# Performance work log

Hardware: AMD Instinct MI355X
Metric: run time of the kernel (lower is better)

## Reference

```python
import jax, jax.numpy as jnp
import numpy as np

B, S, H = 1, 2048, 2048
E, K, I = 8, 2, 1024   # n_routed_experts, num_experts_per_tok, moe_intermediate_size
IS = 2 * I             # shared experts intermediate = moe_intermediate_size * n_shared_experts


def setup_inputs() -> dict:
    key = jax.random.key(0)
    ks = jax.random.split(key, 8)
    w = 0.02  # weight scale so gate softmax is not degenerate
    return {
        "x": jax.random.normal(ks[0], (B, S, H), jnp.float32),
        "gate_w": jax.random.normal(ks[1], (E, H), jnp.float32) * w,
        "wg": jax.random.normal(ks[2], (E, H, I), jnp.float32) * w,
        "wu": jax.random.normal(ks[3], (E, H, I), jnp.float32) * w,
        "wd": jax.random.normal(ks[4], (E, I, H), jnp.float32) * w,
        "sg": jax.random.normal(ks[5], (H, IS), jnp.float32) * w,
        "su": jax.random.normal(ks[6], (H, IS), jnp.float32) * w,
        "sd": jax.random.normal(ks[7], (IS, H), jnp.float32) * w,
    }


def reference(x, gate_w, wg, wu, wd, sg, su, sd):
    b, s, h = x.shape
    xf = x.reshape(-1, h)                                  # [T, H]
    T = xf.shape[0]

    # ---- gate: softmax scores, top-k, renormalize ----
    scores = jax.nn.softmax(jnp.einsum("th,eh->te", xf, gate_w), axis=-1)  # [T, E]
    topk_w, topk_i = jax.lax.top_k(scores, K)              # sorted descending
    topk_w = topk_w / jnp.sum(topk_w, axis=-1, keepdims=True)

    # dense combine weights [T, E] (indices unique per token)
    cw = jnp.zeros_like(scores).at[jnp.arange(T)[:, None], topk_i].add(topk_w)

    # ---- routed experts: SwiGLU MLP per expert, weighted combine ----
    g = jnp.einsum("th,ehi->eti", xf, wg)                  # [E, T, I]
    u = jnp.einsum("th,ehi->eti", xf, wu)
    hgated = jax.nn.silu(g) * u
    eo = jnp.einsum("eti,eih->eth", hgated, wd)            # [E, T, H]
    y = jnp.einsum("te,eth->th", cw, eo)                   # [T, H]

    # ---- shared experts ----
    shared = (jax.nn.silu(xf @ sg) * (xf @ su)) @ sd       # [T, H]

    return (y + shared).reshape(b, s, h)
```

## Files before the change

### kernel.cpp

```cpp
#include <hip/hip_runtime.h>


typedef unsigned short u16;
typedef unsigned int   u32;
typedef __bf16 bf16x8 __attribute__((ext_vector_type(8)));
typedef float  f32x4  __attribute__((ext_vector_type(4)));

#define T_TOK 2048
#define HDIM  2048
#define IDIM  1024
#define NEXP  8
#define ISDIM 2048
#define MAXROWS 5120

__device__ __forceinline__ u16 f2bf(float f) {
  u32 x = __float_as_uint(f);
  return (u16)((x + 0x7FFFu + ((x >> 16) & 1u)) >> 16);
}
__device__ __forceinline__ float bf2f(u16 v) { return __uint_as_float(((u32)v) << 16); }

#define GLL(g, l)                                                              \
  __builtin_amdgcn_global_load_lds(                                            \
      (const __attribute__((address_space(1))) void*)(g),                      \
      (__attribute__((address_space(3))) void*)(l), 16, 0, 0)

__global__ void init_kernel(int* __restrict__ perm, int* __restrict__ meta,
                            int* __restrict__ zrow) {
  int idx = blockIdx.x * 256 + threadIdx.x;
  if (idx < 8192) perm[idx] = -1;
  if (idx < 16) meta[idx] = 0;
  if (idx < 1024) zrow[idx] = 0;
}

__global__ __launch_bounds__(256) void gate_kernel(
    const float* __restrict__ x, const float* __restrict__ gw,
    u16* __restrict__ xb, float* __restrict__ outz,
    float* __restrict__ topw, int* __restrict__ topi, int* __restrict__ meta) {
  const int t = blockIdx.x, tid = threadIdx.x;
  const long o = (long)t * HDIM + tid * 8;
  float4 a = *(const float4*)(x + o);
  float4 b = *(const float4*)(x + o + 4);
  float4 z = {0.f, 0.f, 0.f, 0.f};
  *(float4*)(outz + o) = z;
  *(float4*)(outz + o + 4) = z;
  uint4 w;
  w.x = (u32)f2bf(a.x) | ((u32)f2bf(a.y) << 16);
  w.y = (u32)f2bf(a.z) | ((u32)f2bf(a.w) << 16);
  w.z = (u32)f2bf(b.x) | ((u32)f2bf(b.y) << 16);
  w.w = (u32)f2bf(b.z) | ((u32)f2bf(b.w) << 16);
  *(uint4*)(xb + o) = w;
  float acc[NEXP];
#pragma unroll
  for (int e = 0; e < NEXP; e++) {
    const float* gr = gw + e * HDIM + tid * 8;
    float4 wa = *(const float4*)gr;
    float4 wb = *(const float4*)(gr + 4);
    acc[e] = a.x * wa.x + a.y * wa.y + a.z * wa.z + a.w * wa.w +
             b.x * wb.x + b.y * wb.y + b.z * wb.z + b.w * wb.w;
  }
#pragma unroll
  for (int off = 32; off; off >>= 1)
#pragma unroll
    for (int e = 0; e < NEXP; e++) acc[e] += __shfl_down(acc[e], off, 64);
  __shared__ float red[4][NEXP];
  if ((tid & 63) == 0) {
#pragma unroll
    for (int e = 0; e < NEXP; e++) red[tid >> 6][e] = acc[e];
  }
  __syncthreads();
  if (tid == 0) {
    float s[NEXP];
#pragma unroll
    for (int e = 0; e < NEXP; e++) s[e] = red[0][e] + red[1][e] + red[2][e] + red[3][e];
    int i0 = 0;
#pragma unroll
    for (int e = 1; e < NEXP; e++)
      if (s[e] > s[i0]) i0 = e;
    int i1 = -1;
#pragma unroll
    for (int e = 0; e < NEXP; e++) {
      if (e == i0) continue;
      if (i1 < 0 || s[e] > s[i1]) i1 = e;
    }
    float w0 = 1.f / (1.f + __expf(s[i1] - s[i0]));
    topw[t * 2 + 0] = w0;
    topw[t * 2 + 1] = 1.f - w0;
    topi[t * 2 + 0] = i0;
    topi[t * 2 + 1] = i1;
    atomicAdd(meta + i0, 1);
    atomicAdd(meta + i1, 1);
  }
}

__global__ void scan_kernel(int* __restrict__ meta) {
  if (threadIdx.x == 0 && blockIdx.x == 0) {
    int o = 0;
    meta[16] = 0;
#pragma unroll
    for (int e = 0; e < NEXP; e++) {
      o += (meta[e] + 127) & ~127;
      meta[17 + e] = o;
    }
  }
}

__global__ void assign_kernel(const int* __restrict__ topi, int* __restrict__ meta,
                              int* __restrict__ perm, int* __restrict__ tokrow) {
  int idx = blockIdx.x * 256 + threadIdx.x;
  int e = topi[idx];
  int pos = atomicAdd(meta + 8 + e, 1);
  int row = meta[16 + e] + pos;
  perm[row] = idx;
  tokrow[idx] = row;
}

__device__ __forceinline__ void tcast_tile(const float* __restrict__ in,
                                           u16* __restrict__ out, int R, int C) {
  __shared__ float tile[64 * 65];
  int r0 = blockIdx.y * 64, c0 = blockIdx.x * 64;
  int t = threadIdx.x;
  int i = t >> 4, j4 = t & 15;
#pragma unroll
  for (int ii = 0; ii < 4; ii++) {
    int r = i + ii * 16;
    float4 v = *(const float4*)(in + (long)(r0 + r) * C + c0 + j4 * 4);
    tile[r * 65 + j4 * 4 + 0] = v.x;
    tile[r * 65 + j4 * 4 + 1] = v.y;
    tile[r * 65 + j4 * 4 + 2] = v.z;
    tile[r * 65 + j4 * 4 + 3] = v.w;
  }
  __syncthreads();
  int cc = t >> 3, rr = (t & 7) * 8;
#pragma unroll
  for (int pp = 0; pp < 2; pp++) {
    int c = cc + pp * 32;
    u16 e[8];
#pragma unroll
    for (int u = 0; u < 8; u++) e[u] = f2bf(tile[(rr + u) * 65 + c]);
    uint4 w;
    w.x = (u32)e[0] | ((u32)e[1] << 16);
    w.y = (u32)e[2] | ((u32)e[3] << 16);
    w.z = (u32)e[4] | ((u32)e[5] << 16);
    w.w = (u32)e[6] | ((u32)e[7] << 16);
    *(uint4*)(out + (long)(c0 + c) * R + r0 + rr) = w;
  }
}

__global__ __launch_bounds__(256) void tcast_kernel(const float* __restrict__ in,
                                                    u16* __restrict__ out, int R, int C,
                                                    long inz, long outz) {
  tcast_tile(in + (long)blockIdx.z * inz, out + (long)blockIdx.z * outz, R, C);
}

__global__ __launch_bounds__(256) void tcast2_kernel(
    const float* __restrict__ inA, const float* __restrict__ inB,
    u16* __restrict__ out, int R, int C, long inz, long outz, long boff, int zsplit) {
  int z = blockIdx.z;
  const float* in;
  u16* o;
  if (z < zsplit) {
    in = inA + (long)z * inz;
    o = out + (long)z * outz;
  } else {
    int e = z - zsplit;
    in = inB + (long)e * inz;
    o = out + (long)e * outz + boff;
  }
  tcast_tile(in, o, R, C);
}

template <int HALF8>
__device__ __forceinline__ void silu_do(u16* __restrict__ buf, long i) {
  long r = i / HALF8, c = i % HALF8;
  u16* g = buf + r * (long)HALF8 * 16 + c * 8;
  uint4 gv = *(const uint4*)g;
  uint4 uv = *(const uint4*)(g + HALF8 * 8);
  const u32* gp = &gv.x;
  const u32* up = &uv.x;
  uint4 w;
  u32* wp = &w.x;
#pragma unroll
  for (int j = 0; j < 4; j++) {
    float g0 = bf2f((u16)(gp[j] & 0xFFFF)), g1 = bf2f((u16)(gp[j] >> 16));
    float u0 = bf2f((u16)(up[j] & 0xFFFF)), u1 = bf2f((u16)(up[j] >> 16));
    float r0 = g0 / (1.f + __expf(-g0)) * u0;
    float r1 = g1 / (1.f + __expf(-g1)) * u1;
    wp[j] = (u32)f2bf(r0) | ((u32)f2bf(r1) << 16);
  }
  *(uint4*)g = w;
}

template <int HALF8>
__global__ void silu_kernel(u16* __restrict__ buf) {
  long i = (long)blockIdx.x * 256 + threadIdx.x;
  silu_do<HALF8>(buf, i);
}

__global__ void silu2_kernel(u16* __restrict__ gur, u16* __restrict__ gus) {
  const long NR = (long)MAXROWS * IDIM / 8;
  long i = (long)blockIdx.x * 256 + threadIdx.x;
  if (i < NR)
    silu_do<128>(gur, i);
  else
    silu_do<256>(gus, i - NR);
}

template <int CMODE , bool PERMA, bool SEGB>
__device__ __forceinline__ void gemm_body2(
    int mt, int nt, u16* lds, const u16* __restrict__ A, long lda,
    const u16* __restrict__ B, long ldbz, int K, u16* __restrict__ Cb,
    float* __restrict__ Cf, long ldc, const int* __restrict__ offp,
    const int* __restrict__ perm, const u16* __restrict__ zrow) {
  const int row0 = mt * 128;
  if constexpr (SEGB) {
    if (row0 >= offp[8]) return;
    int e = 0;
    while (offp[e + 1] <= row0) ++e;
    B += (long)e * ldbz;
  }
  const int tid = threadIdx.x;

  const int ra = tid >> 2, sa = tid & 3;
  const u16* gA;
  if constexpr (PERMA) {
    int p = perm[row0 + ra];
    gA = ((p < 0) ? zrow : A + (long)(p >> 1) * lda) + (sa ^ ((ra >> 1) & 3)) * 8;
  } else {
    gA = A + (long)(row0 + ra) * lda + (sa ^ ((ra >> 1) & 3)) * 8;
  }
  const int rb0 = ra, rb1 = ra + 128;
  const u16* gB0 = B + (long)(nt * 256 + rb0) * K + (sa ^ ((rb0 >> 1) & 3)) * 8;
  const u16* gB1 = B + (long)(nt * 256 + rb1) * K + (sa ^ ((rb1 >> 1) & 3)) * 8;
  const int dAo = tid * 8;
  const int dBo = 4096 + tid * 8;

  const int lane = tid & 63, w = tid >> 6;
  const int wm = (w >> 2) * 64, wn = (w & 3) * 64;
  const int lrow = lane & 15, kc = lane >> 4;
  int offA[4], offB[4];
#pragma unroll
  for (int i = 0; i < 4; i++) {
    int rA = wm + i * 16 + lrow;
    offA[i] = rA * 32 + (kc ^ ((rA >> 1) & 3)) * 8;
    int rB = wn + i * 16 + lrow;
    offB[i] = 4096 + rB * 32 + (kc ^ ((rB >> 1) & 3)) * 8;
  }

  f32x4 acc[4][4];
#pragma unroll
  for (int i = 0; i < 4; i++)
#pragma unroll
    for (int j = 0; j < 4; j++) acc[i][j] = f32x4{0.f, 0.f, 0.f, 0.f};

  const int nk = K >> 5;
  {
    u16* b0 = lds;
    GLL(gA, b0 + dAo);
    GLL(gB0, b0 + dBo);
    GLL(gB1, b0 + dBo + 4096);
    u16* b1 = lds + 12288;
    GLL(gA + 32, b1 + dAo);
    GLL(gB0 + 32, b1 + dBo);
    GLL(gB1 + 32, b1 + dBo + 4096);
  }
  int cur = 0, stg = 2;
  for (int t = 0; t < nk; ++t) {
    asm volatile("s_waitcnt vmcnt(3)" ::: "memory");
    __builtin_amdgcn_s_barrier();
    u16* buf = lds + cur * 12288;
    bf16x8 af[4], bfv[4];
#pragma unroll
    for (int i = 0; i < 4; i++) af[i] = *(const bf16x8*)(buf + offA[i]);
#pragma unroll
    for (int i = 0; i < 4; i++) bfv[i] = *(const bf16x8*)(buf + offB[i]);
    int t2 = t + 2;
    if (t2 >= nk) t2 -= nk;
    {
      u16* sb = lds + stg * 12288;
      const int kk = t2 * 32;
      GLL(gA + kk, sb + dAo);
      GLL(gB0 + kk, sb + dBo);
      GLL(gB1 + kk, sb + dBo + 4096);
    }
    __builtin_amdgcn_s_barrier();
    __builtin_amdgcn_s_setprio(1);
#pragma unroll
    for (int mi = 0; mi < 4; mi++)
#pragma unroll
      for (int ni = 0; ni < 4; ni++)
        acc[mi][ni] = __builtin_amdgcn_mfma_f32_16x16x32_bf16(af[mi], bfv[ni],
                                                              acc[mi][ni], 0, 0, 0);
    __builtin_amdgcn_s_setprio(0);
    cur = (cur == 2) ? 0 : cur + 1;
    stg = (stg == 2) ? 0 : stg + 1;
  }
  asm volatile("s_waitcnt vmcnt(0)" ::: "memory");

  const int crow = row0 + wm + ((lane >> 4) << 2);
  const int ccol = nt * 256 + wn + (lane & 15);
#pragma unroll
  for (int mi = 0; mi < 4; mi++) {
#pragma unroll
    for (int ni = 0; ni < 4; ni++) {
#pragma unroll
      for (int r = 0; r < 4; r++) {
        int row = crow + mi * 16 + r;
        int col = ccol + ni * 16;
        float v = acc[mi][ni][r];
        if constexpr (CMODE == 0) {
          Cb[(long)row * ldc + col] = f2bf(v);
        } else {
          Cf[(long)row * ldc + col] = v;
        }
      }
    }
  }
}

__global__ __launch_bounds__(512, 4) void gemm_gu_fused(
    const u16* __restrict__ xb, const u16* __restrict__ wguT,
    const u16* __restrict__ sgsuT, u16* __restrict__ gur, u16* __restrict__ gus,
    const int* __restrict__ offp, const int* __restrict__ perm,
    const u16* __restrict__ zrow) {
  __shared__ __align__(16) u16 lds2[36864];
  int bid = blockIdx.x;
  if (bid < 320) {
    gemm_body2<0, true, true>(bid >> 3, bid & 7, lds2, xb, HDIM, wguT,
                              (long)2 * IDIM * HDIM, HDIM, gur, nullptr, 2 * IDIM,
                              offp, perm, zrow);
  } else {
    int b = bid - 320;
    gemm_body2<0, false, false>(b >> 4, b & 15, lds2, xb, HDIM, sgsuT, 0, HDIM, gus,
                                nullptr, 2 * ISDIM, nullptr, nullptr, nullptr);
  }
}

__global__ __launch_bounds__(512, 4) void gemm_down_plain(
    const u16* __restrict__ gus, const u16* __restrict__ sdT,
    const u16* __restrict__ gur, const u16* __restrict__ wdT, float* __restrict__ out,
    u16* __restrict__ eo, const int* __restrict__ offp) {
  __shared__ __align__(16) u16 lds2[36864];
  int bid = blockIdx.x;
  if (bid < 128) {
    gemm_body2<1, false, false>(bid >> 3, bid & 7, lds2, gus, 2 * ISDIM, sdT, 0, ISDIM,
                                nullptr, out, HDIM, nullptr, nullptr, nullptr);
  } else {
    int b = bid - 128;
    gemm_body2<0, false, true>(b >> 3, b & 7, lds2, gur, 2 * IDIM, wdT,
                               (long)HDIM * IDIM, IDIM, eo, nullptr, HDIM, offp,
                               nullptr, nullptr);
  }
}

__global__ __launch_bounds__(256) void combine_kernel(float* __restrict__ out,
                                                      const u16* __restrict__ eo,
                                                      const int* __restrict__ tokrow,
                                                      const float* __restrict__ topw) {
  const int t = blockIdx.x, tid = threadIdx.x;
  const long o = (long)t * HDIM + tid * 8;
  const int r0 = tokrow[t * 2], r1 = tokrow[t * 2 + 1];
  const float w0 = topw[t * 2], w1 = topw[t * 2 + 1];
  float4 a = *(const float4*)(out + o);
  float4 b = *(const float4*)(out + o + 4);
  uint4 e0 = *(const uint4*)(eo + (long)r0 * HDIM + tid * 8);
  uint4 e1 = *(const uint4*)(eo + (long)r1 * HDIM + tid * 8);
  const u32* p0 = &e0.x;
  const u32* p1 = &e1.x;
  float r[8] = {a.x, a.y, a.z, a.w, b.x, b.y, b.z, b.w};
#pragma unroll
  for (int j = 0; j < 4; j++) {
    r[j * 2 + 0] += w0 * bf2f((u16)(p0[j] & 0xFFFF)) + w1 * bf2f((u16)(p1[j] & 0xFFFF));
    r[j * 2 + 1] += w0 * bf2f((u16)(p0[j] >> 16)) + w1 * bf2f((u16)(p1[j] >> 16));
  }
  float4 oa = {r[0], r[1], r[2], r[3]};
  float4 ob = {r[4], r[5], r[6], r[7]};
  *(float4*)(out + o) = oa;
  *(float4*)(out + o + 4) = ob;
}

template <int CMODE, bool PERMA, bool SEGB>
__device__ __forceinline__ void gemm_body(
    int mt, int nt, u16* ldsA, u16* ldsB, const u16* __restrict__ A, long lda,
    const u16* __restrict__ B, long ldbz, int K, u16* __restrict__ Cb,
    float* __restrict__ Cf, long ldc, const int* __restrict__ offp,
    const int* __restrict__ perm, const float* __restrict__ topw,
    const u16* __restrict__ zrow) {
  const int row0 = mt * 128;
  if constexpr (SEGB) {
    if (row0 >= offp[8]) return;
    int e = 0;
    while (offp[e + 1] <= row0) ++e;
    B += (long)e * ldbz;
  }
  const int tid = threadIdx.x;
  const u16* gA[4];
  const u16* gB[4];
  u16 *lA[4], *lB[4];
#pragma unroll
  for (int j = 0; j < 4; j++) {
    int c = tid + 256 * j;
    int r = c >> 3, s = c & 7;
    int gk = (s ^ (r & 7)) * 8;
    const u16* arow;
    if constexpr (PERMA) {
      int p = perm[row0 + r];
      arow = (p < 0) ? zrow : A + (long)(p >> 1) * lda;
    } else {
      arow = A + (long)(row0 + r) * lda;
    }
    gA[j] = arow + gk;
    gB[j] = B + (long)(nt * 128 + r) * K + gk;
    lA[j] = ldsA + c * 8;
    lB[j] = ldsB + c * 8;
  }
  const int lane = tid & 63, wave = tid >> 6;
  const int wm = (wave & 1) * 64, wn = (wave >> 1) * 64;
  const int lrow = lane & 15;
  const int kchunk = lane >> 4;
  const int rsw = lrow & 7;

  f32x4 acc[4][4];
#pragma unroll
  for (int i = 0; i < 4; i++)
#pragma unroll
    for (int j = 0; j < 4; j++) acc[i][j] = f32x4{0.f, 0.f, 0.f, 0.f};

  const int nk = K >> 6;
  for (int kt = 0; kt < nk; ++kt) {
    const int kk = kt * 64;
#pragma unroll
    for (int j = 0; j < 4; j++) {
      GLL(gA[j] + kk, lA[j]);
      GLL(gB[j] + kk, lB[j]);
    }
    __syncthreads();
#pragma unroll
    for (int half = 0; half < 2; half++) {
      const int slot = (kchunk + half * 4) ^ rsw;
      bf16x8 af[4], bfv[4];
#pragma unroll
      for (int mi = 0; mi < 4; mi++)
        af[mi] = *(const bf16x8*)(ldsA + (wm + lrow + mi * 16) * 64 + slot * 8);
#pragma unroll
      for (int ni = 0; ni < 4; ni++)
        bfv[ni] = *(const bf16x8*)(ldsB + (wn + lrow + ni * 16) * 64 + slot * 8);
#pragma unroll
      for (int mi = 0; mi < 4; mi++)
#pragma unroll
        for (int ni = 0; ni < 4; ni++)
          acc[mi][ni] = __builtin_amdgcn_mfma_f32_16x16x32_bf16(af[mi], bfv[ni],
                                                                acc[mi][ni], 0, 0, 0);
    }
    __syncthreads();
  }

  const int crow = row0 + wm + ((lane >> 4) << 2);
  const int ccol = nt * 128 + wn + (lane & 15);
#pragma unroll
  for (int mi = 0; mi < 4; mi++) {
#pragma unroll
    for (int ni = 0; ni < 4; ni++) {
#pragma unroll
      for (int r = 0; r < 4; r++) {
        int row = crow + mi * 16 + r;
        int col = ccol + ni * 16;
        float v = acc[mi][ni][r];
        if constexpr (CMODE == 0) {
          Cb[(long)row * ldc + col] = f2bf(v);
        } else if constexpr (CMODE == 1) {
          Cf[(long)row * ldc + col] = v;
        } else if constexpr (CMODE == 2) {
          int p = perm[row];
          if (p >= 0) atomicAdd(Cf + (long)(p >> 1) * ldc + col, topw[p] * v);
        } else {
          atomicAdd(Cf + (long)row * ldc + col, v);
        }
      }
    }
  }
}

__global__ __launch_bounds__(256) void gemm_routed_gu(
    const u16* __restrict__ xb, const u16* __restrict__ wT, u16* __restrict__ Cb,
    const int* __restrict__ offp, const int* __restrict__ perm,
    const u16* __restrict__ zrow) {
  __shared__ __align__(16) u16 ldsA[8192], ldsB[8192];
  gemm_body<0, true, true>(blockIdx.y, blockIdx.x, ldsA, ldsB, xb, HDIM, wT,
                           (long)IDIM * HDIM, HDIM, Cb, nullptr, 2 * IDIM, offp, perm,
                           nullptr, zrow);
}
__global__ __launch_bounds__(256) void gemm_shared_gu(const u16* __restrict__ xb,
                                                      const u16* __restrict__ sgsuT,
                                                      u16* __restrict__ gus) {
  __shared__ __align__(16) u16 ldsA[8192], ldsB[8192];
  gemm_body<0, false, false>(blockIdx.y, blockIdx.x, ldsA, ldsB, xb, HDIM, sgsuT, 0, HDIM,
                             gus, nullptr, 2 * ISDIM, nullptr, nullptr, nullptr, nullptr);
}
__global__ __launch_bounds__(256) void gemm_down_atomic(
    const u16* __restrict__ gus, const u16* __restrict__ sdT,
    const u16* __restrict__ gur, const u16* __restrict__ wdT, float* __restrict__ out,
    const int* __restrict__ offp, const int* __restrict__ perm,
    const float* __restrict__ topw) {
  __shared__ __align__(16) u16 ldsA[8192], ldsB[8192];
  int bid = blockIdx.x;
  if (bid < 256) {
    gemm_body<3, false, false>(bid / 16, bid % 16, ldsA, ldsB, gus, 2 * ISDIM, sdT, 0,
                               ISDIM, nullptr, out, HDIM, nullptr, nullptr, nullptr,
                               nullptr);
  } else {
    int b = bid - 256;
    gemm_body<2, false, true>(b / 16, b % 16, ldsA, ldsB, gur, 2 * IDIM, wdT,
                              (long)HDIM * IDIM, IDIM, nullptr, out, HDIM, offp, perm,
                              topw, nullptr);
  }
}

extern "C" void kernel_launch(void* const* d_in, const int* in_sizes, int n_in,
                              void* d_out, int out_size, void* d_ws, size_t ws_size,
                              hipStream_t stream) {
  const float* x  = (const float*)d_in[0];
  const float* gw = (const float*)d_in[1];
  const float* wg = (const float*)d_in[2];
  const float* wu = (const float*)d_in[3];
  const float* wd = (const float*)d_in[4];
  const float* sg = (const float*)d_in[5];
  const float* su = (const float*)d_in[6];
  const float* sd = (const float*)d_in[7];
  float* out = (float*)d_out;

  char* ws = (char*)d_ws;
  size_t off = 0;
  auto alloc = [&](size_t b) {
    size_t o = off;
    off += (b + 255) & ~(size_t)255;
    return (void*)(ws + o);
  };
  u16*   xb     = (u16*)alloc((size_t)T_TOK * HDIM * 2);
  u16*   gur    = (u16*)alloc((size_t)MAXROWS * 2 * IDIM * 2);
  u16*   gus    = (u16*)alloc((size_t)T_TOK * 2 * ISDIM * 2);
  float* topw   = (float*)alloc((size_t)T_TOK * 2 * 4);
  int*   topi   = (int*)alloc((size_t)T_TOK * 2 * 4);
  int*   tokrow = (int*)alloc((size_t)T_TOK * 2 * 4);
  int*   perm   = (int*)alloc(8192 * 4);
  int*   meta   = (int*)alloc(64 * 4);
  u16*   zrow   = (u16*)alloc(4096);
  size_t base = off;

  const size_t SZ_WGUT  = (size_t)NEXP * 2 * IDIM * HDIM * 2;
  const size_t SZ_SGSUT = (size_t)2 * ISDIM * HDIM * 2;
  const size_t SZ_SDT   = (size_t)HDIM * ISDIM * 2;
  const size_t SZ_WDT   = (size_t)NEXP * HDIM * IDIM * 2;
  const bool fused = ws_size >= base + SZ_WGUT + SZ_SGSUT;

  init_kernel<<<32, 256, 0, stream>>>(perm, meta, (int*)zrow);
  gate_kernel<<<T_TOK, 256, 0, stream>>>(x, gw, xb, out, topw, topi, meta);
  scan_kernel<<<1, 64, 0, stream>>>(meta);
  assign_kernel<<<16, 256, 0, stream>>>(topi, meta, perm, tokrow);

  if (fused) {
    u16* wguT  = (u16*)(ws + base);
    u16* sgsuT = (u16*)(ws + base + SZ_WGUT);
    u16* sdT   = wguT;
    u16* wdT   = wguT + SZ_SDT / 2;
    u16* eo    = wguT + (SZ_SDT + SZ_WDT) / 2;
    tcast2_kernel<<<dim3(IDIM / 64, HDIM / 64, 2 * NEXP), 256, 0, stream>>>(
        wg, wu, wguT, HDIM, IDIM, (long)HDIM * IDIM, (long)2 * IDIM * HDIM,
        (long)IDIM * HDIM, NEXP);
    tcast2_kernel<<<dim3(ISDIM / 64, HDIM / 64, 2), 256, 0, stream>>>(
        sg, su, sgsuT, HDIM, ISDIM, 0, 0, (long)ISDIM * HDIM, 1);
    gemm_gu_fused<<<576, 512, 0, stream>>>(xb, wguT, sgsuT, gur, gus, meta + 16, perm,
                                           zrow);
    silu2_kernel<<<(MAXROWS * IDIM / 8 + T_TOK * ISDIM / 8) / 256, 256, 0, stream>>>(
        gur, gus);
    tcast_kernel<<<dim3(HDIM / 64, ISDIM / 64, 1), 256, 0, stream>>>(sd, sdT, ISDIM,
                                                                     HDIM, 0, 0);
    tcast_kernel<<<dim3(HDIM / 64, IDIM / 64, NEXP), 256, 0, stream>>>(
        wd, wdT, IDIM, HDIM, (long)IDIM * HDIM, (long)HDIM * IDIM);
    gemm_down_plain<<<448, 512, 0, stream>>>(gus, sdT, gur, wdT, out, eo, meta + 16);
    combine_kernel<<<T_TOK, 256, 0, stream>>>(out, eo, tokrow, topw);
  } else {
    u16* wT    = (u16*)(ws + base);
    u16* sgsuT = wT;
    u16* sdT   = wT;
    u16* wdT   = wT + SZ_SDT / 2;
    tcast_kernel<<<dim3(IDIM / 64, HDIM / 64, NEXP), 256, 0, stream>>>(
        wg, wT, HDIM, IDIM, (long)HDIM * IDIM, (long)IDIM * HDIM);
    gemm_routed_gu<<<dim3(8, MAXROWS / 128), 256, 0, stream>>>(xb, wT, gur, meta + 16,
                                                               perm, zrow);
    tcast_kernel<<<dim3(IDIM / 64, HDIM / 64, NEXP), 256, 0, stream>>>(
        wu, wT, HDIM, IDIM, (long)HDIM * IDIM, (long)IDIM * HDIM);
    gemm_routed_gu<<<dim3(8, MAXROWS / 128), 256, 0, stream>>>(xb, wT, gur + IDIM,
                                                               meta + 16, perm, zrow);
    silu_kernel<128><<<(MAXROWS * IDIM / 8) / 256, 256, 0, stream>>>(gur);
    tcast_kernel<<<dim3(ISDIM / 64, HDIM / 64, 1), 256, 0, stream>>>(sg, sgsuT, HDIM,
                                                                     ISDIM, 0, 0);
    tcast_kernel<<<dim3(ISDIM / 64, HDIM / 64, 1), 256, 0, stream>>>(
        su, sgsuT + (size_t)ISDIM * HDIM, HDIM, ISDIM, 0, 0);
    gemm_shared_gu<<<dim3(32, 16), 256, 0, stream>>>(xb, sgsuT, gus);
    silu_kernel<256><<<(T_TOK * ISDIM / 8) / 256, 256, 0, stream>>>(gus);
    tcast_kernel<<<dim3(HDIM / 64, ISDIM / 64, 1), 256, 0, stream>>>(sd, sdT, ISDIM,
                                                                     HDIM, 0, 0);
    tcast_kernel<<<dim3(HDIM / 64, IDIM / 64, NEXP), 256, 0, stream>>>(
        wd, wdT, IDIM, HDIM, (long)IDIM * HDIM, (long)HDIM * IDIM);
    gemm_down_atomic<<<896, 256, 0, stream>>>(gus, sdT, gur, wdT, out, meta + 16, perm,
                                              topw);
  }
}
```

Measured before the change: 498.4 us.

## Enlarge GEMM M-tiles to 256/192 rows with split-phase LDS pipelining

```diff
diff --git a/kernel.cpp b/kernel.cpp
--- a/kernel.cpp
+++ b/kernel.cpp
@@ -11,7 +11,8 @@
 #define IDIM  1024
 #define NEXP  8
 #define ISDIM 2048
-#define MAXROWS 5120
+#define MAXROWS   5760
+#define MAXROWS_FB 5120
 
 __device__ __forceinline__ u16 f2bf(float f) {
   u32 x = __float_as_uint(f);
@@ -92,13 +93,13 @@
   }
 }
 
-__global__ void scan_kernel(int* __restrict__ meta) {
+__global__ void scan_kernel(int* __restrict__ meta, int pad) {
   if (threadIdx.x == 0 && blockIdx.x == 0) {
     int o = 0;
     meta[16] = 0;
 #pragma unroll
     for (int e = 0; e < NEXP; e++) {
-      o += (meta[e] + 127) & ~127;
+      o += ((meta[e] + pad - 1) / pad) * pad;
       meta[17 + e] = o;
     }
   }
@@ -205,13 +206,13 @@
     silu_do<256>(gus, i - NR);
 }
 
-template <int CMODE , bool PERMA, bool SEGB>
-__device__ __forceinline__ void gemm_body2(
+template <int CMODE , int MI, bool PERMA, bool SEGB>
+__device__ __forceinline__ void gemm_body3(
     int mt, int nt, u16* lds, const u16* __restrict__ A, long lda,
     const u16* __restrict__ B, long ldbz, int K, u16* __restrict__ Cb,
     float* __restrict__ Cf, long ldc, const int* __restrict__ offp,
     const int* __restrict__ perm, const u16* __restrict__ zrow) {
-  const int row0 = mt * 128;
+  const int row0 = mt * (MI * 32);
   if constexpr (SEGB) {
     if (row0 >= offp[8]) return;
     int e = 0;
@@ -221,76 +222,100 @@
   const int tid = threadIdx.x;
 
   const int ra = tid >> 2, sa = tid & 3;
-  const u16* gA;
+  const int swz0 = (sa ^ ((ra >> 1) & 3)) * 8;
+  const u16 *gA0, *gA1;
   if constexpr (PERMA) {
-    int p = perm[row0 + ra];
-    gA = ((p < 0) ? zrow : A + (long)(p >> 1) * lda) + (sa ^ ((ra >> 1) & 3)) * 8;
+    int p0 = perm[row0 + ra];
+    int p1 = perm[row0 + 128 + ra];
+    gA0 = ((p0 < 0) ? zrow : A + (long)(p0 >> 1) * lda) + swz0;
+    gA1 = ((p1 < 0) ? zrow : A + (long)(p1 >> 1) * lda) + swz0;
   } else {
-    gA = A + (long)(row0 + ra) * lda + (sa ^ ((ra >> 1) & 3)) * 8;
-  }
-  const int rb0 = ra, rb1 = ra + 128;
-  const u16* gB0 = B + (long)(nt * 256 + rb0) * K + (sa ^ ((rb0 >> 1) & 3)) * 8;
-  const u16* gB1 = B + (long)(nt * 256 + rb1) * K + (sa ^ ((rb1 >> 1) & 3)) * 8;
-  const int dAo = tid * 8;
-  const int dBo = 4096 + tid * 8;
+    gA0 = A + (long)(row0 + ra) * lda + swz0;
+    gA1 = A + (long)(row0 + 128 + ra) * lda + swz0;
+  }
+  const u16* gB0 = B + (long)(nt * 256 + ra) * K + swz0;
+  const u16* gB1 = B + (long)(nt * 256 + 128 + ra) * K + swz0;
 
   const int lane = tid & 63, w = tid >> 6;
-  const int wm = (w >> 2) * 64, wn = (w & 3) * 64;
+  const int wm = (w >> 2) * (MI * 16), wn = (w & 3) * 64;
   const int lrow = lane & 15, kc = lane >> 4;
-  int offA[4], offB[4];
+  int offA[MI], offB[4];
+#pragma unroll
+  for (int i = 0; i < MI; i++) {
+    int r = wm + i * 16 + lrow;
+    offA[i] = r * 32 + ((kc ^ ((r >> 1) & 3)) << 3);
+  }
 #pragma unroll
   for (int i = 0; i < 4; i++) {
-    int rA = wm + i * 16 + lrow;
-    offA[i] = rA * 32 + (kc ^ ((rA >> 1) & 3)) * 8;
-    int rB = wn + i * 16 + lrow;
-    offB[i] = 4096 + rB * 32 + (kc ^ ((rB >> 1) & 3)) * 8;
-  }
-
-  f32x4 acc[4][4];
-#pragma unroll
-  for (int i = 0; i < 4; i++)
+    int r = wn + i * 16 + lrow;
+    offB[i] = 8192 + r * 32 + ((kc ^ ((r >> 1) & 3)) << 3);
+  }
+
+  f32x4 acc[MI][4];
+#pragma unroll
+  for (int i = 0; i < MI; i++)
 #pragma unroll
     for (int j = 0; j < 4; j++) acc[i][j] = f32x4{0.f, 0.f, 0.f, 0.f};
 
   const int nk = K >> 5;
   {
     u16* b0 = lds;
-    GLL(gA, b0 + dAo);
-    GLL(gB0, b0 + dBo);
-    GLL(gB1, b0 + dBo + 4096);
-    u16* b1 = lds + 12288;
-    GLL(gA + 32, b1 + dAo);
-    GLL(gB0 + 32, b1 + dBo);
-    GLL(gB1 + 32, b1 + dBo + 4096);
-  }
+    GLL(gA0, b0 + tid * 8);
+    GLL(gA1, b0 + 4096 + tid * 8);
+    GLL(gB0, b0 + 8192 + tid * 8);
+    GLL(gB1, b0 + 12288 + tid * 8);
+    u16* b1 = lds + 16384;
+    GLL(gA0 + 32, b1 + tid * 8);
+    GLL(gA1 + 32, b1 + 4096 + tid * 8);
+    GLL(gB0 + 32, b1 + 8192 + tid * 8);
+    GLL(gB1 + 32, b1 + 12288 + tid * 8);
+  }
+  asm volatile("s_waitcnt vmcnt(4)" ::: "memory");
+  asm volatile("s_barrier" ::: "memory");
+
+  constexpr int MH = MI / 2;
   int cur = 0, stg = 2;
   for (int t = 0; t < nk; ++t) {
-    asm volatile("s_waitcnt vmcnt(3)" ::: "memory");
-    __builtin_amdgcn_s_barrier();
-    u16* buf = lds + cur * 12288;
-    bf16x8 af[4], bfv[4];
-#pragma unroll
-    for (int i = 0; i < 4; i++) af[i] = *(const bf16x8*)(buf + offA[i]);
-#pragma unroll
-    for (int i = 0; i < 4; i++) bfv[i] = *(const bf16x8*)(buf + offB[i]);
     int t2 = t + 2;
     if (t2 >= nk) t2 -= nk;
-    {
-      u16* sb = lds + stg * 12288;
-      const int kk = t2 * 32;
-      GLL(gA + kk, sb + dAo);
-      GLL(gB0 + kk, sb + dBo);
-      GLL(gB1 + kk, sb + dBo + 4096);
-    }
-    __builtin_amdgcn_s_barrier();
+    const int kk2 = t2 * 32;
+    u16* buf = lds + cur * 16384;
+    u16* sb = lds + stg * 16384;
+
+    bf16x8 af[MH], bfv[4];
+#pragma unroll
+    for (int i = 0; i < MH; i++) af[i] = *(const bf16x8*)(buf + offA[i]);
+#pragma unroll
+    for (int i = 0; i < 4; i++) bfv[i] = *(const bf16x8*)(buf + offB[i]);
+    GLL(gA0 + kk2, sb + tid * 8);
+    GLL(gA1 + kk2, sb + 4096 + tid * 8);
+    asm volatile("s_barrier" ::: "memory");
     __builtin_amdgcn_s_setprio(1);
 #pragma unroll
-    for (int mi = 0; mi < 4; mi++)
+    for (int mi = 0; mi < MH; mi++)
 #pragma unroll
       for (int ni = 0; ni < 4; ni++)
         acc[mi][ni] = __builtin_amdgcn_mfma_f32_16x16x32_bf16(af[mi], bfv[ni],
                                                               acc[mi][ni], 0, 0, 0);
     __builtin_amdgcn_s_setprio(0);
+    asm volatile("s_barrier" ::: "memory");
+
+    bf16x8 ag[MI - MH];
+#pragma unroll
+    for (int i = 0; i < MI - MH; i++) ag[i] = *(const bf16x8*)(buf + offA[MH + i]);
+    GLL(gB0 + kk2, sb + 8192 + tid * 8);
+    GLL(gB1 + kk2, sb + 12288 + tid * 8);
+    asm volatile("s_barrier" ::: "memory");
+    __builtin_amdgcn_s_setprio(1);
+#pragma unroll
+    for (int mi = 0; mi < MI - MH; mi++)
+#pragma unroll
+      for (int ni = 0; ni < 4; ni++)
+        acc[MH + mi][ni] = __builtin_amdgcn_mfma_f32_16x16x32_bf16(
+            ag[mi], bfv[ni], acc[MH + mi][ni], 0, 0, 0);
+    __builtin_amdgcn_s_setprio(0);
+    asm volatile("s_waitcnt vmcnt(4)" ::: "memory");
+    asm volatile("s_barrier" ::: "memory");
     cur = (cur == 2) ? 0 : cur + 1;
     stg = (stg == 2) ? 0 : stg + 1;
   }
@@ -299,7 +324,7 @@
   const int crow = row0 + wm + ((lane >> 4) << 2);
   const int ccol = nt * 256 + wn + (lane & 15);
 #pragma unroll
-  for (int mi = 0; mi < 4; mi++) {
+  for (int mi = 0; mi < MI; mi++) {
 #pragma unroll
     for (int ni = 0; ni < 4; ni++) {
 #pragma unroll
@@ -317,38 +342,38 @@
   }
 }
 
-__global__ __launch_bounds__(512, 4) void gemm_gu_fused(
+__global__ __launch_bounds__(512, 2) void gemm_gu_fused(
     const u16* __restrict__ xb, const u16* __restrict__ wguT,
     const u16* __restrict__ sgsuT, u16* __restrict__ gur, u16* __restrict__ gus,
     const int* __restrict__ offp, const int* __restrict__ perm,
     const u16* __restrict__ zrow) {
-  __shared__ __align__(16) u16 lds2[36864];
+  __shared__ __align__(16) u16 lds3[49152];
   int bid = blockIdx.x;
-  if (bid < 320) {
-    gemm_body2<0, true, true>(bid >> 3, bid & 7, lds2, xb, HDIM, wguT,
-                              (long)2 * IDIM * HDIM, HDIM, gur, nullptr, 2 * IDIM,
-                              offp, perm, zrow);
+  if (bid < 128) {
+    gemm_body3<0, 8, false, false>(bid >> 4, bid & 15, lds3, xb, HDIM, sgsuT, 0, HDIM,
+                                   gus, nullptr, 2 * ISDIM, nullptr, nullptr, nullptr);
   } else {
-    int b = bid - 320;
-    gemm_body2<0, false, false>(b >> 4, b & 15, lds2, xb, HDIM, sgsuT, 0, HDIM, gus,
-                                nullptr, 2 * ISDIM, nullptr, nullptr, nullptr);
-  }
-}
-
-__global__ __launch_bounds__(512, 4) void gemm_down_plain(
+    int b = bid - 128;
+    gemm_body3<0, 6, true, true>(b >> 3, b & 7, lds3, xb, HDIM, wguT,
+                                 (long)2 * IDIM * HDIM, HDIM, gur, nullptr, 2 * IDIM,
+                                 offp, perm, zrow);
+  }
+}
+
+__global__ __launch_bounds__(512, 2) void gemm_down_plain(
     const u16* __restrict__ gus, const u16* __restrict__ sdT,
     const u16* __restrict__ gur, const u16* __restrict__ wdT, float* __restrict__ out,
     u16* __restrict__ eo, const int* __restrict__ offp) {
-  __shared__ __align__(16) u16 lds2[36864];
+  __shared__ __align__(16) u16 lds3[49152];
   int bid = blockIdx.x;
-  if (bid < 128) {
-    gemm_body2<1, false, false>(bid >> 3, bid & 7, lds2, gus, 2 * ISDIM, sdT, 0, ISDIM,
-                                nullptr, out, HDIM, nullptr, nullptr, nullptr);
+  if (bid < 64) {
+    gemm_body3<1, 8, false, false>(bid >> 3, bid & 7, lds3, gus, 2 * ISDIM, sdT, 0,
+                                   ISDIM, nullptr, out, HDIM, nullptr, nullptr, nullptr);
   } else {
-    int b = bid - 128;
-    gemm_body2<0, false, true>(b >> 3, b & 7, lds2, gur, 2 * IDIM, wdT,
-                               (long)HDIM * IDIM, IDIM, eo, nullptr, HDIM, offp,
-                               nullptr, nullptr);
+    int b = bid - 64;
+    gemm_body3<0, 6, false, true>(b >> 3, b & 7, lds3, gur, 2 * IDIM, wdT,
+                                  (long)HDIM * IDIM, IDIM, eo, nullptr, HDIM, offp,
+                                  nullptr, nullptr);
   }
 }
 
@@ -554,7 +579,7 @@
 
   init_kernel<<<32, 256, 0, stream>>>(perm, meta, (int*)zrow);
   gate_kernel<<<T_TOK, 256, 0, stream>>>(x, gw, xb, out, topw, topi, meta);
-  scan_kernel<<<1, 64, 0, stream>>>(meta);
+  scan_kernel<<<1, 64, 0, stream>>>(meta, fused ? 192 : 128);
   assign_kernel<<<16, 256, 0, stream>>>(topi, meta, perm, tokrow);
 
   if (fused) {
@@ -568,7 +593,7 @@
         (long)IDIM * HDIM, NEXP);
     tcast2_kernel<<<dim3(ISDIM / 64, HDIM / 64, 2), 256, 0, stream>>>(
         sg, su, sgsuT, HDIM, ISDIM, 0, 0, (long)ISDIM * HDIM, 1);
-    gemm_gu_fused<<<576, 512, 0, stream>>>(xb, wguT, sgsuT, gur, gus, meta + 16, perm,
+    gemm_gu_fused<<<368, 512, 0, stream>>>(xb, wguT, sgsuT, gur, gus, meta + 16, perm,
                                            zrow);
     silu2_kernel<<<(MAXROWS * IDIM / 8 + T_TOK * ISDIM / 8) / 256, 256, 0, stream>>>(
         gur, gus);
@@ -576,7 +601,7 @@
                                                                      HDIM, 0, 0);
     tcast_kernel<<<dim3(HDIM / 64, IDIM / 64, NEXP), 256, 0, stream>>>(
         wd, wdT, IDIM, HDIM, (long)IDIM * HDIM, (long)HDIM * IDIM);
-    gemm_down_plain<<<448, 512, 0, stream>>>(gus, sdT, gur, wdT, out, eo, meta + 16);
+    gemm_down_plain<<<304, 512, 0, stream>>>(gus, sdT, gur, wdT, out, eo, meta + 16);
     combine_kernel<<<T_TOK, 256, 0, stream>>>(out, eo, tokrow, topw);
   } else {
     u16* wT    = (u16*)(ws + base);
@@ -585,13 +610,13 @@
     u16* wdT   = wT + SZ_SDT / 2;
     tcast_kernel<<<dim3(IDIM / 64, HDIM / 64, NEXP), 256, 0, stream>>>(
         wg, wT, HDIM, IDIM, (long)HDIM * IDIM, (long)IDIM * HDIM);
-    gemm_routed_gu<<<dim3(8, MAXROWS / 128), 256, 0, stream>>>(xb, wT, gur, meta + 16,
-                                                               perm, zrow);
+    gemm_routed_gu<<<dim3(8, MAXROWS_FB / 128), 256, 0, stream>>>(xb, wT, gur, meta + 16,
+                                                                  perm, zrow);
     tcast_kernel<<<dim3(IDIM / 64, HDIM / 64, NEXP), 256, 0, stream>>>(
         wu, wT, HDIM, IDIM, (long)HDIM * IDIM, (long)IDIM * HDIM);
-    gemm_routed_gu<<<dim3(8, MAXROWS / 128), 256, 0, stream>>>(xb, wT, gur + IDIM,
-                                                               meta + 16, perm, zrow);
-    silu_kernel<128><<<(MAXROWS * IDIM / 8) / 256, 256, 0, stream>>>(gur);
+    gemm_routed_gu<<<dim3(8, MAXROWS_FB / 128), 256, 0, stream>>>(
+        xb, wT, gur + IDIM, meta + 16, perm, zrow);
+    silu_kernel<128><<<(MAXROWS_FB * IDIM / 8) / 256, 256, 0, stream>>>(gur);
     tcast_kernel<<<dim3(ISDIM / 64, HDIM / 64, 1), 256, 0, stream>>>(sg, sgsuT, HDIM,
                                                                      ISDIM, 0, 0);
     tcast_kernel<<<dim3(ISDIM / 64, HDIM / 64, 1), 256, 0, stream>>>(
```

Measured after the change: 511.4 us. 1.03x slower.
